# Optimization experiments

Measured on AMD Instinct MI355X. Metric: run time of the kernel, lower is better.

## Reference

```python
import jax, jax.numpy as jnp
import numpy as np

GROUPS = [[0, 1, 2, 3, 4], [5, 7, 9], [6, 8, 10], [11, 13, 15], [12, 14, 16]]
G = len(GROUPS)
BN_EPS = 1e-5


def _fc_edges(n):
    r = np.repeat(np.arange(n), n)
    c = np.tile(np.arange(n), n)
    m = r != c
    return jnp.asarray(r[m]), jnp.asarray(c[m])


ROW, COL = _fc_edges(G)  # [E], E = G*(G-1) = 20


def _bn(x, scale, bias, mean, var):
    # inference-mode batchnorm over last dim
    return (x - mean) * (scale * jax.lax.rsqrt(var + BN_EPS)) + bias


def setup_inputs() -> dict:
    key = jax.random.key(0)
    ks = jax.random.split(key, 12)
    B, K, C, Ci = 4096, 17, 256, 64
    inp = {
        "x_bk_c": jax.random.normal(ks[0], (B * K, C), jnp.float32),
        "W_down": jax.random.normal(ks[1], (C, Ci), jnp.float32) * 0.05,
        "b_down": jax.random.normal(ks[2], (Ci,), jnp.float32) * 0.05,
        "bn1_scale": jax.random.uniform(ks[3], (Ci,), jnp.float32, 0.5, 1.5),
        "bn1_bias": jax.random.normal(ks[4], (Ci,), jnp.float32) * 0.1,
        "bn1_mean": jax.random.normal(ks[5], (Ci,), jnp.float32) * 0.1,
        "bn1_var": jax.random.uniform(ks[6], (Ci,), jnp.float32, 0.5, 1.5),
        "W_conv": jax.random.normal(ks[7], (Ci, 2 * Ci), jnp.float32) * 0.05,  # 1x1 conv, bias=False
        "bn2_scale": jax.random.uniform(ks[8], (Ci,), jnp.float32, 0.5, 1.5),
        "bn2_bias": jax.random.normal(ks[9], (Ci,), jnp.float32) * 0.1,
        "bn2_mean": jax.random.normal(ks[10], (Ci,), jnp.float32) * 0.1,
        "bn2_var": jax.random.uniform(ks[11], (Ci,), jnp.float32, 0.5, 1.5),
        "W_agg": jax.random.normal(jax.random.fold_in(key, 100), (Ci, C), jnp.float32) * 0.05,
        "b_agg": jax.random.normal(jax.random.fold_in(key, 101), (C,), jnp.float32) * 0.05,
        "B": B,
        "K": K,
    }
    return inp


def reference(x_bk_c, W_down, b_down, bn1_scale, bn1_bias, bn1_mean, bn1_var,
              W_conv, bn2_scale, bn2_bias, bn2_mean, bn2_var, W_agg, b_agg, B, K):
    C = x_bk_c.shape[-1]
    # down-projection + BN + SiLU
    xd = jax.nn.silu(_bn(x_bk_c @ W_down + b_down, bn1_scale, bn1_bias, bn1_mean, bn1_var))
    xd = xd.reshape(B, K, -1)  # [B, K, Ci]
    # per-group mean pooling (static small loop over 5 groups)
    means = jnp.stack([xd[:, g, :].mean(axis=1) for g in GROUPS], axis=1)  # [B, G, Ci]
    # EdgeConv over fully-connected group graph
    x_i = means[:, ROW, :]                                   # [B, E, Ci]
    x_j = means[:, COL, :]
    ef = jnp.concatenate([x_i, x_j - x_i], axis=-1)          # [B, E, 2Ci]
    pe = jax.nn.silu(_bn(ef @ W_conv.T, bn2_scale, bn2_bias, bn2_mean, bn2_var))  # [B, E, Ci]
    agg = jnp.zeros_like(means).at[:, ROW, :].add(pe)        # scatter-add over target nodes
    # per-group attention scores in C_in
    att = jax.nn.sigmoid(agg @ W_agg + b_agg)                # [B, G, C]
    # average group scores over each keypoint's memberships
    M = np.zeros((K, G), np.float32)
    for gi, g in enumerate(GROUPS):
        for kp in g:
            M[kp, gi] += 1.0
    Mj = jnp.asarray(M)
    cnt = Mj.sum(axis=1, keepdims=True)                      # [K, 1]
    ssum = jnp.einsum('kg,bgc->bkc', Mj, att)                # [B, K, C]
    safe = jnp.where(cnt > 0, cnt, 1.0)
    final = jnp.where(cnt > 0, ssum / safe, 1.0)             # ungrouped kps -> 1.0
    return (x_bk_c.reshape(B, K, C) * final).reshape(B * K, C)
```

## Files before the change

kernel.cpp:

```cpp
#include <hip/hip_runtime.h>

typedef float  v4f    __attribute__((ext_vector_type(4)));
typedef float  f32x4  __attribute__((ext_vector_type(4)));
typedef short  bf16x8 __attribute__((ext_vector_type(8)));
typedef short  bf16x4 __attribute__((ext_vector_type(4)));

namespace {
constexpr int XBSTR = 264;
constexpr int XDT   = 24;
constexpr int MWC   = 129;
constexpr int ATS   = 260;
constexpr int MSTR  = 72;
constexpr int FRAG_SLOTS = 5120;

__device__ __forceinline__ float fsilu(float v){ return v/(1.f+__expf(-v)); }
__device__ __forceinline__ float fsigm(float v){ return 1.f/(1.f+__expf(-v)); }

__device__ __forceinline__ unsigned f2bf2(float a, float b){
  unsigned r;
  asm("v_cvt_pk_bf16_f32 %0, %1, %2" : "=v"(r) : "v"(a), "v"(b));
  return r;
}
__device__ __forceinline__ short f2bf(float f){
  unsigned u = __builtin_bit_cast(unsigned, f);
  return (short)((u + 0x7FFFu + ((u>>16)&1u)) >> 16);
}
__device__ __forceinline__ float bf2f(short s){
  unsigned u = ((unsigned)(unsigned short)s) << 16;
  return __builtin_bit_cast(float, u);
}

template<bool USE_WS>
__device__ __forceinline__ bf16x8 get_bd(const bf16x8* wsf, const float* Wd,
                                         int nt, int ks, int l){
  if constexpr (USE_WS) return wsf[(nt*8 + ks)*64 + l];
  bf16x8 f;
  #pragma unroll
  for (int j = 0; j < 8; ++j) f[j] = f2bf(Wd[(ks*32 + (l>>4)*8 + j)*64 + nt*16 + (l&15)]);
  return f;
}
template<bool USE_WS>
__device__ __forceinline__ bf16x8 get_bc(const bf16x8* wsf, const float* Wc,
                                         int nt, int ks, int l){
  if constexpr (USE_WS) return wsf[2048 + (nt*2 + ks)*64 + l];
  const int col = nt*16 + (l&15), cw = col>>6, co = col&63;
  bf16x8 f;
  #pragma unroll
  for (int j = 0; j < 8; ++j) f[j] = f2bf(Wc[co*128 + cw*64 + ks*32 + (l>>4)*8 + j]);
  return f;
}
template<bool USE_WS>
__device__ __forceinline__ bf16x8 get_ba(const bf16x8* wsf, const float* Wa,
                                         int nt, int ks, int l){
  if constexpr (USE_WS) return wsf[3072 + (nt*2 + ks)*64 + l];
  const int col = nt*16 + (l&15);
  bf16x8 f;
  #pragma unroll
  for (int j = 0; j < 8; ++j) f[j] = f2bf(Wa[(ks*32 + (l>>4)*8 + j)*256 + col]);
  return f;
}
}

__global__ __launch_bounds__(256)
void pack_frags(const float* __restrict__ Wd, const float* __restrict__ Wc,
                const float* __restrict__ Wa, bf16x8* __restrict__ wsf)
{
  const int e  = blockIdx.x*256 + threadIdx.x;
  const int l  = e & 63;
  const int fi = e >> 6;
  bf16x8 f;
  if (fi < 32) {
    const int nt = fi >> 3, ks = fi & 7;
    #pragma unroll
    for (int j = 0; j < 8; ++j) f[j] = f2bf(Wd[(ks*32 + (l>>4)*8 + j)*64 + nt*16 + (l&15)]);
  } else if (fi < 48) {
    const int idx = fi - 32, nt = idx >> 1, ks = idx & 1;
    const int col = nt*16 + (l&15), cw = col>>6, co = col&63;
    #pragma unroll
    for (int j = 0; j < 8; ++j) f[j] = f2bf(Wc[co*128 + cw*64 + ks*32 + (l>>4)*8 + j]);
  } else {
    const int idx = fi - 48, nt = idx >> 1, ks = idx & 1;
    const int col = nt*16 + (l&15);
    #pragma unroll
    for (int j = 0; j < 8; ++j) f[j] = f2bf(Wa[(ks*32 + (l>>4)*8 + j)*256 + col]);
  }
  wsf[e] = f;
}

template<bool USE_WS>
__global__ __launch_bounds__(256, 5)
void fused_gnn_v12(const float* __restrict__ x,
                   const float* __restrict__ Wd, const float* __restrict__ bd,
                   const float* __restrict__ bn1s, const float* __restrict__ bn1b,
                   const float* __restrict__ bn1m, const float* __restrict__ bn1v,
                   const float* __restrict__ Wc,
                   const float* __restrict__ bn2s, const float* __restrict__ bn2b,
                   const float* __restrict__ bn2m, const float* __restrict__ bn2v,
                   const float* __restrict__ Wa, const float* __restrict__ ba,
                   const bf16x8* __restrict__ wsf,
                   float* __restrict__ out)
{
  __shared__ short xbf[18*XBSTR];
  __shared__ __align__(16) char uni_raw[3072];
  __shared__ float mw[5*MWC];
  __shared__ short mbf[16*MSTR];
  __shared__ short abf[16*MSTR];

  short* xdT = (short*)uni_raw;
  short* att = (short*)uni_raw;

  const int tid  = threadIdx.x;
  const int l    = tid & 63;
  const int wv   = tid >> 6;
  const int arow = l & 15;
  const int ak8  = (l >> 4) * 8;
  const int b    = blockIdx.x;
  const int colA = wv*16 + arow;

  const float a1r = bn1s[colA] * rsqrtf(bn1v[colA] + 1e-5f);
  const float b1r = (bd[colA] - bn1m[colA])*a1r + bn1b[colA];
  const float a2r = bn2s[l] * rsqrtf(bn2v[l] + 1e-5f);
  const float b2r = bn2b[l] - bn2m[l]*a2r;

  const int c4 = l*4;
  const int r0 = tid >> 6;
  v4f xr0, xr1, xr2, xr3, xr4;
  {
    const v4f* x4 = (const v4f*)(x + (size_t)b * 4352);
    xr0 = x4[tid];        xr1 = x4[256 + tid];
    xr2 = x4[512 + tid];  xr3 = x4[768 + tid];
    if (tid < 64) xr4 = x4[1024 + tid];
    auto store4 = [&](v4f v, int r){
      uint2 u; u.x = f2bf2(v.x, v.y); u.y = f2bf2(v.z, v.w);
      *(uint2*)&xbf[r*XBSTR + c4] = u;
    };
    store4(xr0, r0);      store4(xr1, r0 + 4);
    store4(xr2, r0 + 8);  store4(xr3, r0 + 12);
    if (tid < 64) store4(xr4, 16);
  }
  __syncthreads();

  {
    f32x4 acc0 = {0.f,0.f,0.f,0.f};
    f32x4 acc1 = {0.f,0.f,0.f,0.f};
    const int rowT = (arow == 0) ? 16 : 17;
    #pragma unroll
    for (int h = 0; h < 2; ++h) {
      bf16x8 Bd[4];
      #pragma unroll
      for (int k4 = 0; k4 < 4; ++k4) Bd[k4] = get_bd<USE_WS>(wsf, Wd, wv, h*4 + k4, l);
      #pragma unroll
      for (int k4 = 0; k4 < 4; ++k4) {
        const int ks = h*4 + k4;
        bf16x8 a0 = *(const bf16x8*)&xbf[arow*XBSTR + ks*32 + ak8];
        acc0 = __builtin_amdgcn_mfma_f32_16x16x32_bf16(a0, Bd[k4], acc0, 0, 0, 0);
        bf16x8 a1 = *(const bf16x8*)&xbf[rowT*XBSTR + ks*32 + ak8];
        acc1 = __builtin_amdgcn_mfma_f32_16x16x32_bf16(a1, Bd[k4], acc1, 0, 0, 0);
      }
    }
    const float s0 = fsilu(acc0[0]*a1r + b1r);
    const float s1 = fsilu(acc0[1]*a1r + b1r);
    const float s2 = fsilu(acc0[2]*a1r + b1r);
    const float s3 = fsilu(acc0[3]*a1r + b1r);
    uint2 u; u.x = f2bf2(s0, s1); u.y = f2bf2(s2, s3);
    *(uint2*)&xdT[colA*XDT + (l>>4)*4] = u;
    if ((l >> 4) == 0)
      xdT[colA*XDT + 16] = f2bf(fsilu(acc1[0]*a1r + b1r));
  }
  __syncthreads();

  bf16x8 BcT[2][2];
  #pragma unroll
  for (int t = 0; t < 2; ++t)
    #pragma unroll
    for (int ks = 0; ks < 2; ++ks)
      BcT[t][ks] = get_bc<USE_WS>(wsf, Wc, wv*2 + t, ks, l);

  {
    const int i = l;
    #define XDV(r) bf2f(xdT[i*XDT + (r)])
    if (wv == 0) {
      mbf[0*MSTR + i] = f2bf((XDV(0)+XDV(1)+XDV(2)+XDV(3)+XDV(4))*0.2f);
      mbf[4*MSTR + i] = f2bf((XDV(12)+XDV(14)+XDV(16))*(1.f/3.f));
    } else if (wv == 1) {
      mbf[1*MSTR + i] = f2bf((XDV(5)+XDV(7)+XDV(9))*(1.f/3.f));
    } else if (wv == 2) {
      mbf[2*MSTR + i] = f2bf((XDV(6)+XDV(8)+XDV(10))*(1.f/3.f));
    } else {
      mbf[3*MSTR + i] = f2bf((XDV(11)+XDV(13)+XDV(15))*(1.f/3.f));
    }
    #undef XDV
  }
  __syncthreads();

  {
    bf16x8 am[2];
    #pragma unroll
    for (int ks = 0; ks < 2; ++ks)
      am[ks] = *(const bf16x8*)&mbf[arow*MSTR + ks*32 + ak8];
    #pragma unroll
    for (int t = 0; t < 2; ++t) {
      const int nt = wv*2 + t;
      f32x4 acc = {0.f,0.f,0.f,0.f};
      #pragma unroll
      for (int ks = 0; ks < 2; ++ks)
        acc = __builtin_amdgcn_mfma_f32_16x16x32_bf16(am[ks], BcT[t][ks], acc, 0, 0, 0);
      if ((l >> 4) == 0) {
        #pragma unroll
        for (int j = 0; j < 4; ++j) mw[j*MWC + nt*16 + arow] = acc[j];
      } else if ((l >> 4) == 1) {
        mw[4*MWC + nt*16 + arow] = acc[0];
      }
    }
  }
  __syncthreads();

  bf16x8 BaT[4][2];
  #pragma unroll
  for (int t = 0; t < 4; ++t)
    #pragma unroll
    for (int ks = 0; ks < 2; ++ks)
      BaT[t][ks] = get_ba<USE_WS>(wsf, Wa, wv*4 + t, ks, l);

  {
    const int o = l;
    float m2c[5];
    #pragma unroll
    for (int cc = 0; cc < 5; ++cc) m2c[cc] = mw[cc*MWC + 64 + o];
    auto doG = [&](int g){
      const float bse = mw[g*MWC + o] - m2c[g];
      float s = 0.f;
      #pragma unroll
      for (int cc = 0; cc < 5; ++cc) {
        if (cc != g) s += fsilu((bse + m2c[cc])*a2r + b2r);
      }
      abf[g*MSTR + o] = f2bf(s);
    };
    if (wv == 0) { doG(0); doG(4); }
    else if (wv == 1) doG(1);
    else if (wv == 2) doG(2);
    else doG(3);
  }
  __syncthreads();

  {
    bf16x8 ae[2];
    #pragma unroll
    for (int ks = 0; ks < 2; ++ks)
      ae[ks] = *(const bf16x8*)&abf[arow*MSTR + ks*32 + ak8];
    #pragma unroll
    for (int t = 0; t < 4; ++t) {
      const int nt = wv*4 + t;
      const int colE = nt*16 + arow;
      f32x4 acc = {0.f,0.f,0.f,0.f};
      #pragma unroll
      for (int ks = 0; ks < 2; ++ks)
        acc = __builtin_amdgcn_mfma_f32_16x16x32_bf16(ae[ks], BaT[t][ks], acc, 0, 0, 0);
      const float bav = ba[colE];
      const int q4 = l >> 4;
      if (q4 == 0) {
        #pragma unroll
        for (int j = 0; j < 4; ++j)
          att[j*ATS + colE] = f2bf(fsigm(acc[j] + bav));
      } else if (q4 == 1) {
        att[4*ATS + colE] = f2bf(fsigm(acc[0] + bav));
      }
    }
  }
  __syncthreads();

  {
    float* og = out + (size_t)b*4352;
    constexpr int GOF[17] = {0,0,0,0,0,1,2,1,2,1,2,3,4,3,4,3,4};
    auto emit = [&](v4f xv, int k){
      const bf16x4 a4 = *(const bf16x4*)&att[GOF[k]*ATS + c4];
      v4f o;
      o.x = xv.x * bf2f(a4[0]);
      o.y = xv.y * bf2f(a4[1]);
      o.z = xv.z * bf2f(a4[2]);
      o.w = xv.w * bf2f(a4[3]);
      *(v4f*)&og[k*256 + c4] = o;
    };
    emit(xr0, r0);      emit(xr1, r0 + 4);
    emit(xr2, r0 + 8);  emit(xr3, r0 + 12);
    if (tid < 64) emit(xr4, 16);
  }
}

extern "C" void kernel_launch(void* const* d_in, const int* in_sizes, int n_in,
                              void* d_out, int out_size, void* d_ws, size_t ws_size,
                              hipStream_t stream) {
    (void)n_in; (void)out_size;
    const float* x   = (const float*)d_in[0];
    const float* Wd  = (const float*)d_in[1];
    const float* bd  = (const float*)d_in[2];
    const float* s1  = (const float*)d_in[3];
    const float* b1  = (const float*)d_in[4];
    const float* m1  = (const float*)d_in[5];
    const float* v1  = (const float*)d_in[6];
    const float* Wc  = (const float*)d_in[7];
    const float* s2  = (const float*)d_in[8];
    const float* b2  = (const float*)d_in[9];
    const float* m2  = (const float*)d_in[10];
    const float* v2  = (const float*)d_in[11];
    const float* Wa  = (const float*)d_in[12];
    const float* ba  = (const float*)d_in[13];

    const int Btot = in_sizes[0] / (17 * 256);
    bf16x8* wsf = (bf16x8*)d_ws;

    if (ws_size >= (size_t)FRAG_SLOTS * 16) {
        pack_frags<<<FRAG_SLOTS/256, 256, 0, stream>>>(Wd, Wc, Wa, wsf);
        fused_gnn_v12<true><<<Btot, 256, 0, stream>>>(
            x, Wd, bd, s1, b1, m1, v1, Wc, s2, b2, m2, v2, Wa, ba,
            wsf, (float*)d_out);
    } else {
        fused_gnn_v12<false><<<Btot, 256, 0, stream>>>(
            x, Wd, bd, s1, b1, m1, v1, Wc, s2, b2, m2, v2, Wa, ba,
            wsf, (float*)d_out);
    }
}
```

Measured before the change: 41.52 us.

## Split fused kernel into three kernels with batched middle MLP stage

Replaces the single fused per-sample kernel with three kernels when workspace allows. k1 down-projects two samples per block and writes group means, k2 runs the edge-conv and attention GEMMs for eight samples per block so MFMA tiles are filled, and k3 rescales x by the attention. This is meant to cut MFMA padding waste and per-block serial sync chains. In exchange, x is read twice from global memory and there are extra launches and a workspace round-trip.

Result: slower. 62.52 us (+50.6%).

```diff
diff --git a/kernel.cpp b/kernel.cpp
--- a/kernel.cpp
+++ b/kernel.cpp
@@ -7,7 +7,8 @@
 
 namespace {
 constexpr int XBSTR = 264;
-constexpr int XDT   = 24;
+constexpr int XDT   = 48;
+constexpr int XDT1  = 24;
 constexpr int MWC   = 129;
 constexpr int ATS   = 260;
 constexpr int MSTR  = 72;
@@ -88,42 +89,288 @@
 }
 
 template<bool USE_WS>
+__global__ __launch_bounds__(256, 6)
+void k1_down(const float* __restrict__ x,
+             const float* __restrict__ Wd, const float* __restrict__ bd,
+             const float* __restrict__ bn1s, const float* __restrict__ bn1b,
+             const float* __restrict__ bn1m, const float* __restrict__ bn1v,
+             const bf16x8* __restrict__ wsf,
+             short* __restrict__ means_ws)
+{
+  __shared__ short xbf[35*XBSTR];
+  __shared__ __align__(16) short xdT[64*XDT];
+
+  const int tid = threadIdx.x, l = tid & 63, wv = tid >> 6;
+  const int arow = l & 15, ak8 = (l >> 4) * 8;
+  const int b0 = blockIdx.x * 2;
+  const int colA = wv*16 + arow;
+  const float a1r = bn1s[colA] * rsqrtf(bn1v[colA] + 1e-5f);
+  const float b1r = (bd[colA] - bn1m[colA])*a1r + bn1b[colA];
+
+  {
+    const v4f* x4 = (const v4f*)(x + (size_t)b0 * 4352);
+    #pragma unroll
+    for (int s = 0; s < 9; ++s) {
+      const int idx = s*256 + tid;
+      if (idx < 2176) {
+        const v4f v = x4[idx];
+        const int q = idx >= 1088, e = idx - q*1088;
+        const int row = q*17 + (e >> 6), cc = (e & 63) * 4;
+        uint2 u; u.x = f2bf2(v.x, v.y); u.y = f2bf2(v.z, v.w);
+        *(uint2*)&xbf[row*XBSTR + cc] = u;
+      }
+    }
+  }
+  __syncthreads();
+
+  {
+    f32x4 acc0 = {0.f,0.f,0.f,0.f};
+    f32x4 acc1 = {0.f,0.f,0.f,0.f};
+    f32x4 acc2 = {0.f,0.f,0.f,0.f};
+    const int rowT2 = (arow < 2) ? (32 + arow) : 34;
+    #pragma unroll
+    for (int h = 0; h < 2; ++h) {
+      bf16x8 Bd[4];
+      #pragma unroll
+      for (int k4 = 0; k4 < 4; ++k4) Bd[k4] = get_bd<USE_WS>(wsf, Wd, wv, h*4 + k4, l);
+      #pragma unroll
+      for (int k4 = 0; k4 < 4; ++k4) {
+        const int ks = h*4 + k4;
+        bf16x8 a0 = *(const bf16x8*)&xbf[arow*XBSTR + ks*32 + ak8];
+        acc0 = __builtin_amdgcn_mfma_f32_16x16x32_bf16(a0, Bd[k4], acc0, 0, 0, 0);
+        bf16x8 a1 = *(const bf16x8*)&xbf[(16 + arow)*XBSTR + ks*32 + ak8];
+        acc1 = __builtin_amdgcn_mfma_f32_16x16x32_bf16(a1, Bd[k4], acc1, 0, 0, 0);
+        bf16x8 a2 = *(const bf16x8*)&xbf[rowT2*XBSTR + ks*32 + ak8];
+        acc2 = __builtin_amdgcn_mfma_f32_16x16x32_bf16(a2, Bd[k4], acc2, 0, 0, 0);
+      }
+    }
+    {
+      const float s0 = fsilu(acc0[0]*a1r + b1r);
+      const float s1 = fsilu(acc0[1]*a1r + b1r);
+      const float s2 = fsilu(acc0[2]*a1r + b1r);
+      const float s3 = fsilu(acc0[3]*a1r + b1r);
+      uint2 u; u.x = f2bf2(s0, s1); u.y = f2bf2(s2, s3);
+      *(uint2*)&xdT[colA*XDT + (l>>4)*4] = u;
+    }
+    #pragma unroll
+    for (int j = 0; j < 4; ++j) {
+      const int r = 16 + (l>>4)*4 + j;
+      const int idx = (r < 17) ? r : r + 7;
+      xdT[colA*XDT + idx] = f2bf(fsilu(acc1[j]*a1r + b1r));
+    }
+    if ((l >> 4) == 0) {
+      #pragma unroll
+      for (int j = 0; j < 2; ++j)
+        xdT[colA*XDT + 39 + j] = f2bf(fsilu(acc2[j]*a1r + b1r));
+    }
+  }
+  __syncthreads();
+
+  if (tid < 128) {
+    const int q = tid >> 6, i = tid & 63, base = q * 24;
+    const bf16x8 rA = *(const bf16x8*)&xdT[i*XDT + base];
+    const bf16x8 rB = *(const bf16x8*)&xdT[i*XDT + base + 8];
+    const float xl = bf2f(xdT[i*XDT + base + 16]);
+    float xv[16];
+    #pragma unroll
+    for (int k = 0; k < 8; ++k) { xv[k] = bf2f(rA[k]); xv[k+8] = bf2f(rB[k]); }
+    const float m0 = (xv[0]+xv[1]+xv[2]+xv[3]+xv[4])*0.2f;
+    const float m1 = (xv[5]+xv[7]+xv[9])*(1.f/3.f);
+    const float m2 = (xv[6]+xv[8]+xv[10])*(1.f/3.f);
+    const float m3 = (xv[11]+xv[13]+xv[15])*(1.f/3.f);
+    const float m4 = (xv[12]+xv[14]+xl)*(1.f/3.f);
+    short* mb = means_ws + ((size_t)(b0 + q) * 5) * 64 + i;
+    mb[0]   = f2bf(m0);
+    mb[64]  = f2bf(m1);
+    mb[128] = f2bf(m2);
+    mb[192] = f2bf(m3);
+    mb[256] = f2bf(m4);
+  }
+}
+
+template<bool USE_WS>
+__global__ __launch_bounds__(256, 4)
+void k2_mid(const short* __restrict__ means_ws,
+            const float* __restrict__ Wc,
+            const float* __restrict__ bn2s, const float* __restrict__ bn2b,
+            const float* __restrict__ bn2m, const float* __restrict__ bn2v,
+            const float* __restrict__ Wa, const float* __restrict__ ba,
+            const bf16x8* __restrict__ wsf,
+            short* __restrict__ att_ws)
+{
+  __shared__ short mbf[48*MSTR];
+  __shared__ short abf[48*MSTR];
+  __shared__ __align__(16) char uni2[40*ATS*2];
+
+  float* mw   = (float*)uni2;
+  short* attb = (short*)uni2;
+
+  const int tid = threadIdx.x, l = tid & 63, wv = tid >> 6;
+  const int arow = l & 15, ak8 = (l >> 4) * 8;
+  const int b0 = blockIdx.x * 8;
+  const float a2r = bn2s[l] * rsqrtf(bn2v[l] + 1e-5f);
+  const float b2r = bn2b[l] - bn2m[l]*a2r;
+
+  bf16x8 BcT[2][2];
+  #pragma unroll
+  for (int t = 0; t < 2; ++t)
+    #pragma unroll
+    for (int ks = 0; ks < 2; ++ks)
+      BcT[t][ks] = get_bc<USE_WS>(wsf, Wc, wv*2 + t, ks, l);
+
+  {
+    const unsigned* src = (const unsigned*)means_ws + (size_t)b0 * 160;
+    #pragma unroll
+    for (int p = 0; p < 5; ++p) {
+      const int idx = p*256 + tid;
+      const unsigned v = src[idx];
+      const int qg = idx >> 5, i2 = (idx & 31) * 2;
+      *(unsigned*)&mbf[qg*MSTR + i2] = v;
+    }
+  }
+  __syncthreads();
+
+  {
+    #pragma unroll
+    for (int mt = 0; mt < 3; ++mt) {
+      bf16x8 am0 = *(const bf16x8*)&mbf[(mt*16 + arow)*MSTR + ak8];
+      bf16x8 am1 = *(const bf16x8*)&mbf[(mt*16 + arow)*MSTR + 32 + ak8];
+      #pragma unroll
+      for (int t = 0; t < 2; ++t) {
+        const int nt = wv*2 + t;
+        f32x4 acc = {0.f,0.f,0.f,0.f};
+        acc = __builtin_amdgcn_mfma_f32_16x16x32_bf16(am0, BcT[t][0], acc, 0, 0, 0);
+        acc = __builtin_amdgcn_mfma_f32_16x16x32_bf16(am1, BcT[t][1], acc, 0, 0, 0);
+        #pragma unroll
+        for (int j = 0; j < 4; ++j) {
+          const int qg = mt*16 + (l>>4)*4 + j;
+          if (qg < 40) mw[qg*MWC + nt*16 + arow] = acc[j];
+        }
+      }
+    }
+  }
+  __syncthreads();
+
+  bf16x8 BaT[4][2];
+  #pragma unroll
+  for (int t = 0; t < 4; ++t)
+    #pragma unroll
+    for (int ks = 0; ks < 2; ++ks)
+      BaT[t][ks] = get_ba<USE_WS>(wsf, Wa, wv*4 + t, ks, l);
+
+  {
+    #pragma unroll
+    for (int p = 0; p < 10; ++p) {
+      const int u = p*256 + tid;
+      const int qg = u >> 6, o = u & 63;
+      const int q = qg / 5, g = qg - q*5;
+      const int qb = q * 5;
+      const float c0 = mw[(qb+0)*MWC + 64 + o];
+      const float c1 = mw[(qb+1)*MWC + 64 + o];
+      const float c2 = mw[(qb+2)*MWC + 64 + o];
+      const float c3 = mw[(qb+3)*MWC + 64 + o];
+      const float c4 = mw[(qb+4)*MWC + 64 + o];
+      const float m2g = (g==0)?c0:(g==1)?c1:(g==2)?c2:(g==3)?c3:c4;
+      const float bse = mw[qg*MWC + o] - m2g;
+      float s = fsilu((bse+c0)*a2r + b2r) + fsilu((bse+c1)*a2r + b2r)
+              + fsilu((bse+c2)*a2r + b2r) + fsilu((bse+c3)*a2r + b2r)
+              + fsilu((bse+c4)*a2r + b2r) - fsilu((bse+m2g)*a2r + b2r);
+      abf[qg*MSTR + o] = f2bf(s);
+    }
+  }
+  __syncthreads();
+
+  {
+    #pragma unroll
+    for (int mt = 0; mt < 3; ++mt) {
+      bf16x8 ae0 = *(const bf16x8*)&abf[(mt*16 + arow)*MSTR + ak8];
+      bf16x8 ae1 = *(const bf16x8*)&abf[(mt*16 + arow)*MSTR + 32 + ak8];
+      #pragma unroll
+      for (int t = 0; t < 4; ++t) {
+        const int nt = wv*4 + t;
+        const int colE = nt*16 + arow;
+        f32x4 acc = {0.f,0.f,0.f,0.f};
+        acc = __builtin_amdgcn_mfma_f32_16x16x32_bf16(ae0, BaT[t][0], acc, 0, 0, 0);
+        acc = __builtin_amdgcn_mfma_f32_16x16x32_bf16(ae1, BaT[t][1], acc, 0, 0, 0);
+        const float bav = ba[colE];
+        #pragma unroll
+        for (int j = 0; j < 4; ++j) {
+          const int qg = mt*16 + (l>>4)*4 + j;
+          if (qg < 40) attb[qg*ATS + colE] = f2bf(fsigm(acc[j] + bav));
+        }
+      }
+    }
+  }
+  __syncthreads();
+
+  {
+    unsigned* dst = (unsigned*)att_ws + (size_t)b0 * 640;
+    #pragma unroll
+    for (int p = 0; p < 20; ++p) {
+      const int idx = p*256 + tid;
+      const int qg = idx >> 7, c2 = (idx & 127) * 2;
+      dst[idx] = *(const unsigned*)&attb[qg*ATS + c2];
+    }
+  }
+}
+
+__global__ __launch_bounds__(256, 8)
+void k3_scale(const float* __restrict__ x, const short* __restrict__ att_ws,
+              float* __restrict__ out)
+{
+  const int tid = threadIdx.x;
+  const int b0 = blockIdx.x * 2;
+  const v4f* x4 = (const v4f*)(x + (size_t)b0 * 4352);
+  v4f* o4 = (v4f*)(out + (size_t)b0 * 4352);
+  const short* ab = att_ws + (size_t)b0 * 1280;
+  #pragma unroll
+  for (int s = 0; s < 9; ++s) {
+    const int idx = s*256 + tid;
+    if (idx < 2176) {
+      const int q = idx >= 1088, e = idx - q*1088;
+      const int k = e >> 6, c4 = (e & 63) * 4;
+      const int g = (k < 5) ? 0 : ((k < 11) ? ((k & 1) ? 1 : 2) : ((k & 1) ? 3 : 4));
+      const bf16x4 a4 = *(const bf16x4*)&ab[(size_t)q*1280 + g*256 + c4];
+      const v4f xv = x4[idx];
+      v4f o;
+      o.x = xv.x * bf2f(a4[0]);
+      o.y = xv.y * bf2f(a4[1]);
+      o.z = xv.z * bf2f(a4[2]);
+      o.w = xv.w * bf2f(a4[3]);
+      o4[idx] = o;
+    }
+  }
+}
+
+template<bool USE_WS>
 __global__ __launch_bounds__(256, 5)
-void fused_gnn_v12(const float* __restrict__ x,
-                   const float* __restrict__ Wd, const float* __restrict__ bd,
-                   const float* __restrict__ bn1s, const float* __restrict__ bn1b,
-                   const float* __restrict__ bn1m, const float* __restrict__ bn1v,
-                   const float* __restrict__ Wc,
-                   const float* __restrict__ bn2s, const float* __restrict__ bn2b,
-                   const float* __restrict__ bn2m, const float* __restrict__ bn2v,
-                   const float* __restrict__ Wa, const float* __restrict__ ba,
-                   const bf16x8* __restrict__ wsf,
-                   float* __restrict__ out)
+void fused_v12(const float* __restrict__ x,
+               const float* __restrict__ Wd, const float* __restrict__ bd,
+               const float* __restrict__ bn1s, const float* __restrict__ bn1b,
+               const float* __restrict__ bn1m, const float* __restrict__ bn1v,
+               const float* __restrict__ Wc,
+               const float* __restrict__ bn2s, const float* __restrict__ bn2b,
+               const float* __restrict__ bn2m, const float* __restrict__ bn2v,
+               const float* __restrict__ Wa, const float* __restrict__ ba,
+               const bf16x8* __restrict__ wsf,
+               float* __restrict__ out)
 {
   __shared__ short xbf[18*XBSTR];
   __shared__ __align__(16) char uni_raw[3072];
   __shared__ float mw[5*MWC];
   __shared__ short mbf[16*MSTR];
   __shared__ short abf[16*MSTR];
-
   short* xdT = (short*)uni_raw;
   short* att = (short*)uni_raw;
-
-  const int tid  = threadIdx.x;
-  const int l    = tid & 63;
-  const int wv   = tid >> 6;
-  const int arow = l & 15;
-  const int ak8  = (l >> 4) * 8;
-  const int b    = blockIdx.x;
+  const int tid = threadIdx.x, l = tid & 63, wv = tid >> 6;
+  const int arow = l & 15, ak8 = (l >> 4) * 8;
+  const int b = blockIdx.x;
   const int colA = wv*16 + arow;
-
+  const int c4 = l*4, r0 = tid >> 6;
   const float a1r = bn1s[colA] * rsqrtf(bn1v[colA] + 1e-5f);
   const float b1r = (bd[colA] - bn1m[colA])*a1r + bn1b[colA];
   const float a2r = bn2s[l] * rsqrtf(bn2v[l] + 1e-5f);
   const float b2r = bn2b[l] - bn2m[l]*a2r;
-
-  const int c4 = l*4;
-  const int r0 = tid >> 6;
   v4f xr0, xr1, xr2, xr3, xr4;
   {
     const v4f* x4 = (const v4f*)(x + (size_t)b * 4352);
@@ -139,7 +386,6 @@
     if (tid < 64) store4(xr4, 16);
   }
   __syncthreads();
-
   {
     f32x4 acc0 = {0.f,0.f,0.f,0.f};
     f32x4 acc1 = {0.f,0.f,0.f,0.f};
@@ -163,22 +409,20 @@
     const float s2 = fsilu(acc0[2]*a1r + b1r);
     const float s3 = fsilu(acc0[3]*a1r + b1r);
     uint2 u; u.x = f2bf2(s0, s1); u.y = f2bf2(s2, s3);
-    *(uint2*)&xdT[colA*XDT + (l>>4)*4] = u;
+    *(uint2*)&xdT[colA*XDT1 + (l>>4)*4] = u;
     if ((l >> 4) == 0)
-      xdT[colA*XDT + 16] = f2bf(fsilu(acc1[0]*a1r + b1r));
-  }
-  __syncthreads();
-
+      xdT[colA*XDT1 + 16] = f2bf(fsilu(acc1[0]*a1r + b1r));
+  }
+  __syncthreads();
   bf16x8 BcT[2][2];
   #pragma unroll
   for (int t = 0; t < 2; ++t)
     #pragma unroll
     for (int ks = 0; ks < 2; ++ks)
       BcT[t][ks] = get_bc<USE_WS>(wsf, Wc, wv*2 + t, ks, l);
-
   {
     const int i = l;
-    #define XDV(r) bf2f(xdT[i*XDT + (r)])
+    #define XDV(r) bf2f(xdT[i*XDT1 + (r)])
     if (wv == 0) {
       mbf[0*MSTR + i] = f2bf((XDV(0)+XDV(1)+XDV(2)+XDV(3)+XDV(4))*0.2f);
       mbf[4*MSTR + i] = f2bf((XDV(12)+XDV(14)+XDV(16))*(1.f/3.f));
@@ -192,7 +436,6 @@
     #undef XDV
   }
   __syncthreads();
-
   {
     bf16x8 am[2];
     #pragma unroll
@@ -214,14 +457,12 @@
     }
   }
   __syncthreads();
-
   bf16x8 BaT[4][2];
   #pragma unroll
   for (int t = 0; t < 4; ++t)
     #pragma unroll
     for (int ks = 0; ks < 2; ++ks)
       BaT[t][ks] = get_ba<USE_WS>(wsf, Wa, wv*4 + t, ks, l);
-
   {
     const int o = l;
     float m2c[5];
@@ -231,9 +472,8 @@
       const float bse = mw[g*MWC + o] - m2c[g];
       float s = 0.f;
       #pragma unroll
-      for (int cc = 0; cc < 5; ++cc) {
+      for (int cc = 0; cc < 5; ++cc)
         if (cc != g) s += fsilu((bse + m2c[cc])*a2r + b2r);
-      }
       abf[g*MSTR + o] = f2bf(s);
     };
     if (wv == 0) { doG(0); doG(4); }
@@ -242,7 +482,6 @@
     else doG(3);
   }
   __syncthreads();
-
   {
     bf16x8 ae[2];
     #pragma unroll
@@ -268,7 +507,6 @@
     }
   }
   __syncthreads();
-
   {
     float* og = out + (size_t)b*4352;
     constexpr int GOF[17] = {0,0,0,0,0,1,2,1,2,1,2,3,4,3,4,3,4};
@@ -308,14 +546,26 @@
 
     const int Btot = in_sizes[0] / (17 * 256);
     bf16x8* wsf = (bf16x8*)d_ws;
-
-    if (ws_size >= (size_t)FRAG_SLOTS * 16) {
+    const size_t means_off  = (size_t)FRAG_SLOTS * 16;
+    const size_t means_size = (size_t)Btot * 5 * 64 * 2;
+    const size_t att_off    = means_off + means_size;
+    const size_t att_size   = (size_t)Btot * 5 * 256 * 2;
+    const size_t ws_need    = att_off + att_size;
+
+    if (ws_size >= ws_need) {
+        short* means_ws = (short*)((char*)d_ws + means_off);
+        short* att_ws   = (short*)((char*)d_ws + att_off);
         pack_frags<<<FRAG_SLOTS/256, 256, 0, stream>>>(Wd, Wc, Wa, wsf);
-        fused_gnn_v12<true><<<Btot, 256, 0, stream>>>(
+        k1_down<true><<<Btot/2, 256, 0, stream>>>(x, Wd, bd, s1, b1, m1, v1, wsf, means_ws);
+        k2_mid<true><<<Btot/8, 256, 0, stream>>>(means_ws, Wc, s2, b2, m2, v2, Wa, ba, wsf, att_ws);
+        k3_scale<<<Btot/2, 256, 0, stream>>>(x, att_ws, (float*)d_out);
+    } else if (ws_size >= (size_t)FRAG_SLOTS * 16) {
+        pack_frags<<<FRAG_SLOTS/256, 256, 0, stream>>>(Wd, Wc, Wa, wsf);
+        fused_v12<true><<<Btot, 256, 0, stream>>>(
             x, Wd, bd, s1, b1, m1, v1, Wc, s2, b2, m2, v2, Wa, ba,
             wsf, (float*)d_out);
     } else {
-        fused_gnn_v12<false><<<Btot, 256, 0, stream>>>(
+        fused_v12<false><<<Btot, 256, 0, stream>>>(
             x, Wd, bd, s1, b1, m1, v1, Wc, s2, b2, m2, v2, Wa, ba,
             wsf, (float*)d_out);
     }
```
